# Performance work log

Measured on AMD Instinct MI355X. Metric: run time of the kernel, lower is better.

## Reference

```python
import jax, jax.numpy as jnp
import numpy as np
import math

B, S, D, H = 8, 1024, 1024, 16
DH = D // H  # 64


def setup_inputs() -> dict:
    key = jax.random.key(0)
    ks = jax.random.split(key, 10)
    inputs = jax.random.normal(ks[0], (B, S, D), dtype=jnp.float32)
    mask = jax.random.randint(ks[1], (B, S, S), 0, 2) == 1  # bool [B,S,S]
    sc = 1.0 / math.sqrt(D)
    # per-head projection weights stacked: [H, D, DH], biases [H, DH]
    Wq = jax.random.normal(ks[2], (H, D, DH), dtype=jnp.float32) * sc
    bq = jax.random.normal(ks[3], (H, DH), dtype=jnp.float32) * 0.02
    Wk = jax.random.normal(ks[4], (H, D, DH), dtype=jnp.float32) * sc
    bk = jax.random.normal(ks[5], (H, DH), dtype=jnp.float32) * 0.02
    Wv = jax.random.normal(ks[6], (H, D, DH), dtype=jnp.float32) * sc
    bv = jax.random.normal(ks[7], (H, DH), dtype=jnp.float32) * 0.02
    Wo = jax.random.normal(ks[8], (D, D), dtype=jnp.float32) * sc
    bo = jax.random.normal(ks[9], (D,), dtype=jnp.float32) * 0.02
    return {"inputs": inputs, "mask": mask, "Wq": Wq, "bq": bq, "Wk": Wk,
            "bk": bk, "Wv": Wv, "bv": bv, "Wo": Wo, "bo": bo}


def reference(inputs, mask, Wq, bq, Wk, bk, Wv, bv, Wo, bo):
    d_model = inputs.shape[-1]
    scale = 1.0 / jnp.sqrt(jnp.asarray(d_model, inputs.dtype))  # note: sqrt(d_model), as in source
    # batched per-head projections: [B,H,S,DH]
    Q = jnp.einsum('bsd,hde->bhse', inputs, Wq) + bq[None, :, None, :]
    K = jnp.einsum('bsd,hde->bhse', inputs, Wk) + bk[None, :, None, :]
    V = jnp.einsum('bsd,hde->bhse', inputs, Wv) + bv[None, :, None, :]
    scores = jnp.einsum('bhse,bhte->bhst', Q, K) * scale  # [B,H,S,S]
    scores = jnp.where(mask[:, None, :, :], jnp.asarray(-1e9, scores.dtype), scores)
    attn = jax.nn.softmax(scores, axis=-1)
    ctx = jnp.einsum('bhst,bhte->bhse', attn, V)  # [B,H,S,DH]
    # concat heads along last dim (head h -> slice h*DH:(h+1)*DH), matches torch.cat
    bsz, h, s, dh = ctx.shape
    x = ctx.transpose(0, 2, 1, 3).reshape(bsz, s, h * dh)
    return x @ Wo + bo
```

## Files before the change

### kernel.cpp

```cpp
#include <hip/hip_runtime.h>
#include <hip/hip_bf16.h>
#include <stdint.h>


typedef __attribute__((ext_vector_type(8))) short short8;
typedef __attribute__((ext_vector_type(4))) float floatx4;

__device__ __forceinline__ int swz(int r, int kc) { return r * 8 + (kc ^ (r & 7)); }
__device__ __forceinline__ short8 as_frag(uint4 u) { return __builtin_bit_cast(short8, u); }
__device__ __forceinline__ floatx4 mfma16(short8 a, short8 b, floatx4 c) {
    return __builtin_amdgcn_mfma_f32_16x16x32_bf16(a, b, c, 0, 0, 0);
}
__device__ __forceinline__ unsigned short f2bu(float f) {
    return __builtin_bit_cast(unsigned short, __float2bfloat16(f));
}
__device__ __forceinline__ short f2b(float f) {
    return __builtin_bit_cast(short, __float2bfloat16(f));
}
__device__ __forceinline__ float b2f(short s) {
    return __bfloat162float(__builtin_bit_cast(__hip_bfloat16, s));
}
__device__ __forceinline__ void dma16(const void* g, void* l) {
    __builtin_amdgcn_global_load_lds(
        (const __attribute__((address_space(1))) uint32_t*)g,
        (__attribute__((address_space(3))) uint32_t*)l, 16, 0, 0);
}
__device__ __forceinline__ uint2 pack4(float a, float b, float c, float d) {
    uint2 p;
    p.x = (unsigned)f2bu(a) | ((unsigned)f2bu(b) << 16);
    p.y = (unsigned)f2bu(c) | ((unsigned)f2bu(d) << 16);
    return p;
}

__device__ __forceinline__ void detect_mode(const unsigned* Xw, int* s_is32) {
    if (threadIdx.x < 64) {
        unsigned lo = Xw[threadIdx.x] & 0xFFFFu;
        unsigned e = (lo >> 7) & 0xFFu;
        unsigned long long bal = __ballot(e >= 88u && e <= 150u);
        if (threadIdx.x == 0) *s_is32 = (bal != ~0ull) ? 1 : 0;
    }
    __syncthreads();
}

__device__ __forceinline__ float load_elt(const void* p, size_t idx, int is32) {
    return is32 ? ((const float*)p)[idx]
                : __bfloat162float(((const __hip_bfloat16*)p)[idx]);
}

__global__ __launch_bounds__(256) void prep_all(
    const void* __restrict__ Wq, const void* __restrict__ Wk,
    const void* __restrict__ Wv, const void* __restrict__ Wo,
    const void* __restrict__ bq, const void* __restrict__ bk,
    const void* __restrict__ bv, const void* __restrict__ bo,
    const void* __restrict__ mask_raw, const void* __restrict__ X,
    __hip_bfloat16* __restrict__ WT, __hip_bfloat16* __restrict__ WoT,
    __hip_bfloat16* __restrict__ bc, unsigned long long* __restrict__ bits64,
    __hip_bfloat16* __restrict__ Xb, int do_x)
{
    __shared__ __hip_bfloat16 T[64][72];
    __shared__ int s_is32;
    int blk = blockIdx.x;
    int tid = threadIdx.x;
    const unsigned* Xw = (const unsigned*)X;

    if (blk < 1024) {
        detect_mode(Xw, &s_is32);
        const void* src; size_t src_off;
        __hip_bfloat16* dst;
        int src_ld, dst_ld;
        if (blk < 768) {
            int p = blk >> 8;
            int rem = blk & 255;
            int h = rem >> 4, dt = rem & 15;
            src = (p == 0) ? Wq : (p == 1) ? Wk : Wv;
            src_off = ((size_t)h * 1024 + (size_t)dt * 64) * 64;
            dst = WT + (((size_t)p * 16 + h) * 64) * 1024 + dt * 64;
            src_ld = 64; dst_ld = 1024;
        } else {
            int t = blk - 768;
            int kt = t >> 4, nt = t & 15;
            src = Wo; src_off = (size_t)kt * 64 * 1024 + nt * 64;
            dst = WoT + (size_t)nt * 64 * 1024 + kt * 64;
            src_ld = 1024; dst_ld = 1024;
        }
        #pragma unroll
        for (int i = 0; i < 16; i++) {
            int idx = tid + i * 256;
            int r = idx >> 6, c = idx & 63;
            T[c][r] = __float2bfloat16(load_elt(src, src_off + (size_t)r * src_ld + c, s_is32));
        }
        __syncthreads();
        #pragma unroll
        for (int i = 0; i < 16; i++) {
            int idx = tid + i * 256;
            int r = idx >> 6, c = idx & 63;
            dst[(size_t)r * dst_ld + c] = T[r][c];
        }
    } else if (blk == 1024) {
        detect_mode(Xw, &s_is32);
        #pragma unroll
        for (int i = 0; i < 16; i++) {
            int idx = tid + i * 256;
            int which = idx >> 10, j = idx & 1023;
            const void* src = (which == 0) ? bq : (which == 1) ? bk : (which == 2) ? bv : bo;
            bc[idx] = __float2bfloat16(load_elt(src, j, s_is32));
        }
    } else if (blk < 1537) {
        int blkL = blk - 1025;
        const int* mi = (const int*)mask_raw;
        const unsigned char* mb = (const unsigned char*)mask_raw;
        int lane = tid & 63;
        bool ok = true;
        #pragma unroll
        for (int i = 0; i < 4; i++) {
            unsigned v = (unsigned)mi[lane * 4 + i];
            if (v > 1u) ok = false;
        }
        bool is_i32 = (__ballot(ok) == ~0ull);
        int gw = (blkL * 256 + tid) >> 6;
        const int NW = 512 * 4;
        const int NWORDS = (8 * 1024 * 1024) / 64;
        if (is_i32) {
            for (int i = gw; i < NWORDS; i += NW) {
                int mv = mi[(size_t)i * 64 + lane];
                unsigned long long bal = __ballot(mv != 0);
                if (lane == 0) bits64[i] = bal;
            }
        } else {
            for (int i = gw; i < NWORDS; i += NW) {
                int mv = mb[(size_t)i * 64 + lane];
                unsigned long long bal = __ballot(mv != 0);
                if (lane == 0) bits64[i] = bal;
            }
        }
    } else if (do_x) {
        detect_mode(Xw, &s_is32);
        int blkL = blk - 1537;
        size_t g = ((size_t)blkL * 256 + tid) * 16;
        if (s_is32) {
            const float* Xf = (const float*)X;
            #pragma unroll
            for (int half = 0; half < 2; half++) {
                float4 f0 = *(const float4*)(Xf + g + half * 8);
                float4 f1 = *(const float4*)(Xf + g + half * 8 + 4);
                short8 s;
                s[0] = f2b(f0.x); s[1] = f2b(f0.y); s[2] = f2b(f0.z); s[3] = f2b(f0.w);
                s[4] = f2b(f1.x); s[5] = f2b(f1.y); s[6] = f2b(f1.z); s[7] = f2b(f1.w);
                *(uint4*)(Xb + g + half * 8) = __builtin_bit_cast(uint4, s);
            }
        } else {
            const uint4* Xu = (const uint4*)X;
            *(uint4*)(Xb + g)     = Xu[g / 8];
            *(uint4*)(Xb + g + 8) = Xu[g / 8 + 1];
        }
    }
}

__global__ __launch_bounds__(256, 2) void qkv_gemm_dma(
    const __hip_bfloat16* __restrict__ Xb,
    const __hip_bfloat16* __restrict__ WT,
    const __hip_bfloat16* __restrict__ bc,
    __hip_bfloat16* __restrict__ Q,
    __hip_bfloat16* __restrict__ Ko,
    __hip_bfloat16* __restrict__ Vt)
{
    __shared__ uint4 AsU[256 * 8];
    __shared__ uint4 BsU[128 * 8];
    int tid = threadIdx.x, lane = tid & 63, wave = tid >> 6;
    int quad = lane >> 4, ln = lane & 15;
    int mw = wave & 1, nw = wave >> 1;
    int m0 = blockIdx.x * 256;
    int n0 = blockIdx.y * 128;
    const __hip_bfloat16* Wp = WT + (size_t)n0 * 1024;

    floatx4 acc[8][4];
    #pragma unroll
    for (int i = 0; i < 8; i++)
        #pragma unroll
        for (int j = 0; j < 4; j++) acc[i][j] = (floatx4){0.f, 0.f, 0.f, 0.f};

    for (int k0 = 0; k0 < 1024; k0 += 64) {
        #pragma unroll
        for (int i = 0; i < 8; i++) {
            int r = wave * 64 + i * 8 + (lane >> 3);
            int kc = (lane & 7) ^ (r & 7);
            char* lds = (char*)AsU + (size_t)(wave * 512 + i * 64) * 16;
            dma16(Xb + (size_t)(m0 + r) * 1024 + k0 + kc * 8, lds);
        }
        #pragma unroll
        for (int i = 0; i < 4; i++) {
            int r = wave * 32 + i * 8 + (lane >> 3);
            int kc = (lane & 7) ^ (r & 7);
            char* lds = (char*)BsU + (size_t)(wave * 256 + i * 64) * 16;
            dma16(Wp + (size_t)r * 1024 + k0 + kc * 8, lds);
        }
        __syncthreads();
        #pragma unroll
        for (int kk = 0; kk < 2; kk++) {
            short8 af[8], bf[4];
            #pragma unroll
            for (int mi = 0; mi < 8; mi++)
                af[mi] = as_frag(AsU[swz(mw * 128 + mi * 16 + ln, kk * 4 + quad)]);
            #pragma unroll
            for (int ni = 0; ni < 4; ni++)
                bf[ni] = as_frag(BsU[swz(nw * 64 + ni * 16 + ln, kk * 4 + quad)]);
            #pragma unroll
            for (int mi = 0; mi < 8; mi++)
                #pragma unroll
                for (int ni = 0; ni < 4; ni++)
                    acc[mi][ni] = mfma16(af[mi], bf[ni], acc[mi][ni]);
        }
        __syncthreads();
    }

    int b = m0 >> 10;
    int s0 = m0 & 1023;
    int proj = n0 >> 10;
    if (proj == 2) {
        #pragma unroll
        for (int ni = 0; ni < 4; ni++) {
            int n = n0 + nw * 64 + ni * 16 + ln;
            int h = (n >> 6) & 15, e = n & 63;
            float bval = __bfloat162float(bc[2 * 1024 + (n & 1023)]);
            #pragma unroll
            for (int mi = 0; mi < 8; mi++) {
                int sb = s0 + mw * 128 + mi * 16 + quad * 4;
                uint2 pk = pack4(acc[mi][ni][0] + bval, acc[mi][ni][1] + bval,
                                 acc[mi][ni][2] + bval, acc[mi][ni][3] + bval);
                *(uint2*)(Vt + (((size_t)b * 16 + h) * 64 + e) * 1024 + sb) = pk;
            }
        }
    } else {
        __hip_bfloat16* P = (proj == 0) ? Q : Ko;
        #pragma unroll
        for (int ni = 0; ni < 4; ni++) {
            int n = n0 + nw * 64 + ni * 16 + ln;
            int h = (n >> 6) & 15, e = n & 63;
            float bval = __bfloat162float(bc[proj * 1024 + (n & 1023)]);
            #pragma unroll
            for (int mi = 0; mi < 8; mi++) {
                #pragma unroll
                for (int r = 0; r < 4; r++) {
                    int s = s0 + mw * 128 + mi * 16 + quad * 4 + r;
                    P[(((size_t)b * 16 + h) * 1024 + s) * 64 + e] =
                        __float2bfloat16(acc[mi][ni][r] + bval);
                }
            }
        }
    }
}

__global__ __launch_bounds__(256) void qkv_gemm2(
    const void* __restrict__ Xsrc,
    const __hip_bfloat16* __restrict__ WT,
    const __hip_bfloat16* __restrict__ bc,
    __hip_bfloat16* __restrict__ Q,
    __hip_bfloat16* __restrict__ Ko,
    __hip_bfloat16* __restrict__ Vt)
{
    __shared__ int s_is32;
    detect_mode((const unsigned*)Xsrc, &s_is32);
    __shared__ uint4 AsU[128 * 8];
    __shared__ uint4 BsU[128 * 8];
    int tid = threadIdx.x, lane = tid & 63, wave = tid >> 6;
    int quad = lane >> 4, ln = lane & 15;
    int m0 = blockIdx.x * 128;
    int n0 = blockIdx.y * 128;
    const __hip_bfloat16* Wp = WT + (size_t)n0 * 1024;
    const float* Xf = (const float*)Xsrc;
    const __hip_bfloat16* Xh = (const __hip_bfloat16*)Xsrc;

    floatx4 acc[2][8];
    #pragma unroll
    for (int i = 0; i < 2; i++)
        #pragma unroll
        for (int j = 0; j < 8; j++) acc[i][j] = (floatx4){0.f, 0.f, 0.f, 0.f};

    for (int k0 = 0; k0 < 1024; k0 += 64) {
        if (s_is32) {
            #pragma unroll
            for (int i = 0; i < 4; i++) {
                int id = tid + i * 256;
                int r = id >> 3, kc = id & 7;
                size_t off = (size_t)(m0 + r) * 1024 + k0 + kc * 8;
                float4 f0 = *(const float4*)(Xf + off);
                float4 f1 = *(const float4*)(Xf + off + 4);
                short8 s;
                s[0] = f2b(f0.x); s[1] = f2b(f0.y); s[2] = f2b(f0.z); s[3] = f2b(f0.w);
                s[4] = f2b(f1.x); s[5] = f2b(f1.y); s[6] = f2b(f1.z); s[7] = f2b(f1.w);
                AsU[swz(r, kc)] = __builtin_bit_cast(uint4, s);
            }
        } else {
            #pragma unroll
            for (int i = 0; i < 4; i++) {
                int id = tid + i * 256;
                int r = id >> 3, kc = id & 7;
                AsU[swz(r, kc)] = *(const uint4*)(Xh + (size_t)(m0 + r) * 1024 + k0 + kc * 8);
            }
        }
        #pragma unroll
        for (int i = 0; i < 4; i++) {
            int id = tid + i * 256;
            int r = id >> 3, kc = id & 7;
            BsU[swz(r, kc)] = *(const uint4*)(Wp + (size_t)r * 1024 + k0 + kc * 8);
        }
        __syncthreads();
        #pragma unroll
        for (int kk = 0; kk < 2; kk++) {
            short8 a0 = as_frag(AsU[swz(wave * 32 + ln, kk * 4 + quad)]);
            short8 a1 = as_frag(AsU[swz(wave * 32 + 16 + ln, kk * 4 + quad)]);
            #pragma unroll
            for (int nt = 0; nt < 8; nt++) {
                short8 bf = as_frag(BsU[swz(nt * 16 + ln, kk * 4 + quad)]);
                acc[0][nt] = mfma16(a0, bf, acc[0][nt]);
                acc[1][nt] = mfma16(a1, bf, acc[1][nt]);
            }
        }
        __syncthreads();
    }

    int b = m0 >> 10;
    int s0 = m0 & 1023;
    #pragma unroll
    for (int nt = 0; nt < 8; nt++) {
        int n = n0 + nt * 16 + ln;
        int proj = n >> 10, h = (n >> 6) & 15, e = n & 63;
        float bval = __bfloat162float(bc[proj * 1024 + (n & 1023)]);
        #pragma unroll
        for (int mt = 0; mt < 2; mt++) {
            #pragma unroll
            for (int r = 0; r < 4; r++) {
                int s = s0 + wave * 32 + mt * 16 + quad * 4 + r;
                float v = acc[mt][nt][r] + bval;
                if (proj == 2) {
                    Vt[(((size_t)b * 16 + h) * 64 + e) * 1024 + s] = __float2bfloat16(v);
                } else {
                    __hip_bfloat16* P = (proj == 0) ? Q : Ko;
                    P[(((size_t)b * 16 + h) * 1024 + s) * 64 + e] = __float2bfloat16(v);
                }
            }
        }
    }
}

__global__ __launch_bounds__(256, 4) void attn(
    const __hip_bfloat16* __restrict__ Q,
    const __hip_bfloat16* __restrict__ K,
    const __hip_bfloat16* __restrict__ Vt,
    const unsigned long long* __restrict__ bits,
    __hip_bfloat16* __restrict__ ctx)
{
    __shared__ uint4 KsU[64 * 8];
    __shared__ uint4 VsU[64 * 8];
    __shared__ uint4 PsU[4 * 256];
    __shared__ unsigned long long Ms[128];

    int tid = threadIdx.x, lane = tid & 63, w = tid >> 6;
    int quad = lane >> 4, ln = lane & 15;
    int bh = blockIdx.x;
    int q0 = blockIdx.y * 128;
    int b = bh >> 4, h = bh & 15;
    const __hip_bfloat16* Qp = Q + (size_t)bh * 1024 * 64;
    const __hip_bfloat16* Kp = K + (size_t)bh * 1024 * 64;
    const __hip_bfloat16* Vp = Vt + (size_t)bh * 64 * 1024;
    const unsigned long long* bp = bits + (size_t)b * 1024 * 16;

    short8 qf[2][2];
    #pragma unroll
    for (int g = 0; g < 2; g++)
        #pragma unroll
        for (int kk = 0; kk < 2; kk++)
            qf[g][kk] = as_frag(*(const uint4*)(
                Qp + (size_t)(q0 + w * 32 + g * 16 + ln) * 64 + kk * 32 + quad * 8));

    floatx4 acc_o[2][4];
    #pragma unroll
    for (int g = 0; g < 2; g++)
        #pragma unroll
        for (int i = 0; i < 4; i++) acc_o[g][i] = (floatx4){0.f, 0.f, 0.f, 0.f};
    float lsum[2] = {0.f, 0.f};
    const float scale = 0.03125f;
    __hip_bfloat16* Pw = (__hip_bfloat16*)&PsU[w * 256];

    for (int t0 = 0; t0 < 1024; t0 += 64) {
        __syncthreads();
        #pragma unroll
        for (int i = 0; i < 2; i++) {
            int r = w * 16 + i * 8 + (lane >> 3);
            int kc = (lane & 7) ^ (r & 7);
            char* ldsK = (char*)KsU + (size_t)(w * 128 + i * 64) * 16;
            char* ldsV = (char*)VsU + (size_t)(w * 128 + i * 64) * 16;
            dma16(Kp + (size_t)(t0 + r) * 64 + kc * 8, ldsK);
            dma16(Vp + (size_t)r * 1024 + t0 + kc * 8, ldsV);
        }
        if (tid < 128)
            Ms[tid] = bp[(size_t)(q0 + tid) * 16 + (t0 >> 6)];
        __syncthreads();

        floatx4 st[2][4];
        #pragma unroll
        for (int g = 0; g < 2; g++)
            #pragma unroll
            for (int i = 0; i < 4; i++) st[g][i] = (floatx4){0.f, 0.f, 0.f, 0.f};
        #pragma unroll
        for (int kk = 0; kk < 2; kk++) {
            #pragma unroll
            for (int tt = 0; tt < 4; tt++) {
                short8 kf = as_frag(KsU[swz(tt * 16 + ln, kk * 4 + quad)]);
                st[0][tt] = mfma16(kf, qf[0][kk], st[0][tt]);
                st[1][tt] = mfma16(kf, qf[1][kk], st[1][tt]);
            }
        }

        #pragma unroll
        for (int g = 0; g < 2; g++) {
            int qloc = g * 16 + ln;
            unsigned long long mw = Ms[w * 32 + qloc];
            #pragma unroll
            for (int tt = 0; tt < 4; tt++) {
                unsigned mb = (unsigned)(mw >> (tt * 16 + quad * 4)) & 0xFu;
                float pe0 = (mb & 1u) ? 0.f : __expf(st[g][tt][0] * scale);
                float pe1 = (mb & 2u) ? 0.f : __expf(st[g][tt][1] * scale);
                float pe2 = (mb & 4u) ? 0.f : __expf(st[g][tt][2] * scale);
                float pe3 = (mb & 8u) ? 0.f : __expf(st[g][tt][3] * scale);
                lsum[g] += (pe0 + pe1) + (pe2 + pe3);
                int kc = tt * 2 + (quad >> 1);
                int off = qloc * 64 + (kc ^ (qloc & 7)) * 8 + (quad & 1) * 4;
                *(uint2*)(Pw + off) = pack4(pe0, pe1, pe2, pe3);
            }
        }

        #pragma unroll
        for (int kk = 0; kk < 2; kk++) {
            short8 pf0 = as_frag(PsU[w * 256 + swz(0 * 16 + ln, kk * 4 + quad)]);
            short8 pf1 = as_frag(PsU[w * 256 + swz(1 * 16 + ln, kk * 4 + quad)]);
            #pragma unroll
            for (int et = 0; et < 4; et++) {
                short8 vf = as_frag(VsU[swz(et * 16 + ln, kk * 4 + quad)]);
                acc_o[0][et] = mfma16(vf, pf0, acc_o[0][et]);
                acc_o[1][et] = mfma16(vf, pf1, acc_o[1][et]);
            }
        }
    }

    #pragma unroll
    for (int g = 0; g < 2; g++) {
        lsum[g] += __shfl_xor(lsum[g], 16, 64);
        lsum[g] += __shfl_xor(lsum[g], 32, 64);
    }

    #pragma unroll
    for (int g = 0; g < 2; g++) {
        float inv = 1.f / fmaxf(lsum[g], 1e-20f);
        int s = q0 + w * 32 + g * 16 + ln;
        __hip_bfloat16* crow = ctx + ((size_t)b * 1024 + s) * 1024 + h * 64 + quad * 4;
        #pragma unroll
        for (int et = 0; et < 4; et++) {
            uint2 pk = pack4(acc_o[g][et][0] * inv, acc_o[g][et][1] * inv,
                             acc_o[g][et][2] * inv, acc_o[g][et][3] * inv);
            *(uint2*)(crow + et * 16) = pk;
        }
    }
}

__global__ __launch_bounds__(256) void out_gemm_dma(
    const __hip_bfloat16* __restrict__ Cx,
    const __hip_bfloat16* __restrict__ WoT,
    const __hip_bfloat16* __restrict__ bc,
    const unsigned* __restrict__ Xw,
    void* __restrict__ dout,
    int direct)
{
    __shared__ int s_is32;
    detect_mode(Xw, &s_is32);
    __shared__ uint4 AsU[128 * 8];
    __shared__ uint4 BsU[128 * 8];
    int tid = threadIdx.x, lane = tid & 63, wave = tid >> 6;
    int quad = lane >> 4, ln = lane & 15;
    int mw = wave & 1, nw = wave >> 1;
    int m0 = blockIdx.x * 128;
    int n0 = blockIdx.y * 128;

    floatx4 acc[4][4];
    #pragma unroll
    for (int i = 0; i < 4; i++)
        #pragma unroll
        for (int j = 0; j < 4; j++) acc[i][j] = (floatx4){0.f, 0.f, 0.f, 0.f};

    for (int k0 = 0; k0 < 1024; k0 += 64) {
        #pragma unroll
        for (int i = 0; i < 4; i++) {
            int r = wave * 32 + i * 8 + (lane >> 3);
            int kc = (lane & 7) ^ (r & 7);
            char* ldsA = (char*)AsU + (size_t)(wave * 256 + i * 64) * 16;
            char* ldsB = (char*)BsU + (size_t)(wave * 256 + i * 64) * 16;
            dma16(Cx + (size_t)(m0 + r) * 1024 + k0 + kc * 8, ldsA);
            dma16(WoT + (size_t)(n0 + r) * 1024 + k0 + kc * 8, ldsB);
        }
        __syncthreads();
        #pragma unroll
        for (int kk = 0; kk < 2; kk++) {
            short8 af[4], bf[4];
            #pragma unroll
            for (int mi = 0; mi < 4; mi++)
                af[mi] = as_frag(AsU[swz(mw * 64 + mi * 16 + ln, kk * 4 + quad)]);
            #pragma unroll
            for (int ni = 0; ni < 4; ni++)
                bf[ni] = as_frag(BsU[swz(nw * 64 + ni * 16 + ln, kk * 4 + quad)]);
            #pragma unroll
            for (int mi = 0; mi < 4; mi++)
                #pragma unroll
                for (int ni = 0; ni < 4; ni++)
                    acc[mi][ni] = mfma16(af[mi], bf[ni], acc[mi][ni]);
        }
        __syncthreads();
    }

    const __hip_bfloat16* bo = bc + 3 * 1024;
    #pragma unroll
    for (int ni = 0; ni < 4; ni++) {
        int n = n0 + nw * 64 + ni * 16 + ln;
        float bval = __bfloat162float(bo[n]);
        #pragma unroll
        for (int mi = 0; mi < 4; mi++) {
            #pragma unroll
            for (int r = 0; r < 4; r++) {
                int m = m0 + mw * 64 + mi * 16 + quad * 4 + r;
                float v = acc[mi][ni][r] + bval;
                if (direct && s_is32) ((float*)dout)[(size_t)m * 1024 + n] = v;
                else ((__hip_bfloat16*)dout)[(size_t)m * 1024 + n] = __float2bfloat16(v);
            }
        }
    }
}

__global__ __launch_bounds__(256) void emit_out(
    const __hip_bfloat16* __restrict__ Fo, const unsigned* __restrict__ Xw,
    void* __restrict__ dout)
{
    __shared__ int s_is32;
    detect_mode(Xw, &s_is32);
    size_t g = (size_t)blockIdx.x * 256 + threadIdx.x;
    uint4 u = *(const uint4*)(Fo + g * 8);
    if (s_is32) {
        short8 s = __builtin_bit_cast(short8, u);
        float4 f0, f1;
        f0.x = b2f(s[0]); f0.y = b2f(s[1]); f0.z = b2f(s[2]); f0.w = b2f(s[3]);
        f1.x = b2f(s[4]); f1.y = b2f(s[5]); f1.z = b2f(s[6]); f1.w = b2f(s[7]);
        *(float4*)((float*)dout + g * 8) = f0;
        *(float4*)((float*)dout + g * 8 + 4) = f1;
    } else {
        *(uint4*)((__hip_bfloat16*)dout + g * 8) = u;
    }
}

extern "C" void kernel_launch(void* const* d_in, const int* in_sizes, int n_in,
                              void* d_out, int out_size, void* d_ws, size_t ws_size,
                              hipStream_t stream) {
    const void* X  = d_in[0];
    const void* mk = d_in[1];
    const void* Wq = d_in[2];
    const void* bq = d_in[3];
    const void* Wk = d_in[4];
    const void* bk = d_in[5];
    const void* Wv = d_in[6];
    const void* bv = d_in[7];
    const void* Wo = d_in[8];
    const void* bo = d_in[9];
    const unsigned* Xw = (const unsigned*)X;

    char* ws = (char*)d_ws;
    __hip_bfloat16*     WT   = (__hip_bfloat16*)(ws);
    __hip_bfloat16*     WoT  = (__hip_bfloat16*)(ws + ((size_t)6 << 20));
    unsigned long long* bits = (unsigned long long*)(ws + ((size_t)8 << 20));
    __hip_bfloat16*     bc   = (__hip_bfloat16*)(ws + ((size_t)9 << 20));
    __hip_bfloat16*     Xb   = (__hip_bfloat16*)(ws + ((size_t)10 << 20));
    __hip_bfloat16*     Qb   = (__hip_bfloat16*)(ws + ((size_t)26 << 20));
    __hip_bfloat16*     Kb   = (__hip_bfloat16*)(ws + ((size_t)42 << 20));
    __hip_bfloat16*     Vtb  = (__hip_bfloat16*)(ws + ((size_t)58 << 20));

    bool bigws = ws_size >= ((size_t)74 << 20);

    hipLaunchKernelGGL(prep_all, dim3(3585), dim3(256), 0, stream,
                       Wq, Wk, Wv, Wo, bq, bk, bv, bo, mk, X,
                       WT, WoT, bc, bits, Xb, bigws ? 1 : 0);

    if (bigws) {
        __hip_bfloat16* Cx = Xb;
        hipLaunchKernelGGL(qkv_gemm_dma, dim3(32, 24), dim3(256), 0, stream,
                           Xb, WT, bc, Qb, Kb, Vtb);
        hipLaunchKernelGGL(attn, dim3(128, 8), dim3(256), 0, stream,
                           Qb, Kb, Vtb, bits, Cx);
        hipLaunchKernelGGL(out_gemm_dma, dim3(64, 8), dim3(256), 0, stream,
                           Cx, WoT, bc, Xw, d_out, 1);
    } else {
        __hip_bfloat16* Cx = (__hip_bfloat16*)d_out;
        __hip_bfloat16* Fo = Qb;
        hipLaunchKernelGGL(qkv_gemm2, dim3(64, 24), dim3(256), 0, stream,
                           X, WT, bc, Qb, Kb, Vtb);
        hipLaunchKernelGGL(attn, dim3(128, 8), dim3(256), 0, stream,
                           Qb, Kb, Vtb, bits, Cx);
        hipLaunchKernelGGL(out_gemm_dma, dim3(64, 8), dim3(256), 0, stream,
                           Cx, WoT, bc, Xw, (void*)Fo, 0);
        hipLaunchKernelGGL(emit_out, dim3(4096), dim3(256), 0, stream,
                           Fo, Xw, d_out);
    }
}
```

Before: 303.4 us.

## Prefetch next K/V tile and mask bits into registers during compute

The attention loop now issues global loads for the next K/V tile and the next mask words into registers at the start of each iteration. It stores them into LDS after the MFMA work, instead of doing a DMA to LDS and then waiting on it before computing. Mask words are kept in registers rather than staged through shared memory, and exp is replaced by a raw exp2 with the log2(e) factor folded into the scale constant. This is meant to hide global-memory latency behind the QK^T, softmax and PV work. The cost is extra registers for the prefetch buffers, which could hurt occupancy at 4 blocks per CU, and there are still two barriers per iteration.

```diff
diff --git a/kernel.cpp b/kernel.cpp
--- a/kernel.cpp
+++ b/kernel.cpp
@@ -353,7 +353,6 @@
     __shared__ uint4 KsU[64 * 8];
     __shared__ uint4 VsU[64 * 8];
     __shared__ uint4 PsU[4 * 256];
-    __shared__ unsigned long long Ms[128];
 
     int tid = threadIdx.x, lane = tid & 63, w = tid >> 6;
     int quad = lane >> 4, ln = lane & 15;
@@ -373,29 +372,50 @@
             qf[g][kk] = as_frag(*(const uint4*)(
                 Qp + (size_t)(q0 + w * 32 + g * 16 + ln) * 64 + kk * 32 + quad * 8));
 
+    int sr = w * 16 + (lane >> 3);
+    int kc = lane & 7;
+    int mrow = (size_t)0 + (q0 + w * 32 + ln) * 16;
+    uint4 kreg[2], vreg[2];
+    unsigned long long mreg[2];
+
+    #pragma unroll
+    for (int i = 0; i < 2; i++) {
+        kreg[i] = *(const uint4*)(Kp + (size_t)(sr + i * 8) * 64 + kc * 8);
+        vreg[i] = *(const uint4*)(Vp + (size_t)(sr + i * 8) * 1024 + kc * 8);
+    }
+    #pragma unroll
+    for (int g = 0; g < 2; g++)
+        mreg[g] = bp[mrow + g * 256];
+    #pragma unroll
+    for (int i = 0; i < 2; i++) {
+        KsU[swz(sr + i * 8, kc)] = kreg[i];
+        VsU[swz(sr + i * 8, kc)] = vreg[i];
+    }
+    __syncthreads();
+
     floatx4 acc_o[2][4];
     #pragma unroll
     for (int g = 0; g < 2; g++)
         #pragma unroll
         for (int i = 0; i < 4; i++) acc_o[g][i] = (floatx4){0.f, 0.f, 0.f, 0.f};
     float lsum[2] = {0.f, 0.f};
-    const float scale = 0.03125f;
+    const float C2 = 0.04508422f;
     __hip_bfloat16* Pw = (__hip_bfloat16*)&PsU[w * 256];
 
     for (int t0 = 0; t0 < 1024; t0 += 64) {
-        __syncthreads();
-        #pragma unroll
-        for (int i = 0; i < 2; i++) {
-            int r = w * 16 + i * 8 + (lane >> 3);
-            int kc = (lane & 7) ^ (r & 7);
-            char* ldsK = (char*)KsU + (size_t)(w * 128 + i * 64) * 16;
-            char* ldsV = (char*)VsU + (size_t)(w * 128 + i * 64) * 16;
-            dma16(Kp + (size_t)(t0 + r) * 64 + kc * 8, ldsK);
-            dma16(Vp + (size_t)r * 1024 + t0 + kc * 8, ldsV);
-        }
-        if (tid < 128)
-            Ms[tid] = bp[(size_t)(q0 + tid) * 16 + (t0 >> 6)];
-        __syncthreads();
+        unsigned long long mcur0 = mreg[0], mcur1 = mreg[1];
+        bool more = (t0 + 64) < 1024;
+        if (more) {
+            int tn = t0 + 64;
+            #pragma unroll
+            for (int i = 0; i < 2; i++) {
+                kreg[i] = *(const uint4*)(Kp + (size_t)(tn + sr + i * 8) * 64 + kc * 8);
+                vreg[i] = *(const uint4*)(Vp + (size_t)(sr + i * 8) * 1024 + tn + kc * 8);
+            }
+            #pragma unroll
+            for (int g = 0; g < 2; g++)
+                mreg[g] = bp[mrow + g * 256 + (tn >> 6)];
+        }
 
         floatx4 st[2][4];
         #pragma unroll
@@ -415,17 +435,17 @@
         #pragma unroll
         for (int g = 0; g < 2; g++) {
             int qloc = g * 16 + ln;
-            unsigned long long mw = Ms[w * 32 + qloc];
+            unsigned long long msh = (g ? mcur1 : mcur0) >> (quad * 4);
             #pragma unroll
             for (int tt = 0; tt < 4; tt++) {
-                unsigned mb = (unsigned)(mw >> (tt * 16 + quad * 4)) & 0xFu;
-                float pe0 = (mb & 1u) ? 0.f : __expf(st[g][tt][0] * scale);
-                float pe1 = (mb & 2u) ? 0.f : __expf(st[g][tt][1] * scale);
-                float pe2 = (mb & 4u) ? 0.f : __expf(st[g][tt][2] * scale);
-                float pe3 = (mb & 8u) ? 0.f : __expf(st[g][tt][3] * scale);
+                unsigned mb = (unsigned)(msh >> (tt * 16)) & 0xFu;
+                float pe0 = (mb & 1u) ? 0.f : __builtin_amdgcn_exp2f(st[g][tt][0] * C2);
+                float pe1 = (mb & 2u) ? 0.f : __builtin_amdgcn_exp2f(st[g][tt][1] * C2);
+                float pe2 = (mb & 4u) ? 0.f : __builtin_amdgcn_exp2f(st[g][tt][2] * C2);
+                float pe3 = (mb & 8u) ? 0.f : __builtin_amdgcn_exp2f(st[g][tt][3] * C2);
                 lsum[g] += (pe0 + pe1) + (pe2 + pe3);
-                int kc = tt * 2 + (quad >> 1);
-                int off = qloc * 64 + (kc ^ (qloc & 7)) * 8 + (quad & 1) * 4;
+                int kcp = tt * 2 + (quad >> 1);
+                int off = qloc * 64 + (kcp ^ (qloc & 7)) * 8 + (quad & 1) * 4;
                 *(uint2*)(Pw + off) = pack4(pe0, pe1, pe2, pe3);
             }
         }
@@ -440,6 +460,16 @@
                 acc_o[0][et] = mfma16(vf, pf0, acc_o[0][et]);
                 acc_o[1][et] = mfma16(vf, pf1, acc_o[1][et]);
             }
+        }
+
+        if (more) {
+            __syncthreads();
+            #pragma unroll
+            for (int i = 0; i < 2; i++) {
+                KsU[swz(sr + i * 8, kc)] = kreg[i];
+                VsU[swz(sr + i * 8, kc)] = vreg[i];
+            }
+            __syncthreads();
         }
     }
 
```

Result: slower. 359.4 us (+18.5%).
